# Performance work log

Hardware: AMD Instinct MI355X
Metric: run time of the kernel (lower is better)

## Reference

```python
import jax, jax.numpy as jnp
import numpy as np

N_NODES = 16384
N_EDGES = 131072
N_GRAPHS = 64
DIMS = [396, 4096, 2048, 1024, 1024, 2048, 256, 1]  # layer widths from __init__
BN_EPS = 1e-5


def setup_inputs() -> dict:
    key = jax.random.key(0)
    ks = jax.random.split(key, 32)
    inp = {
        "x": jax.random.normal(ks[0], (N_NODES, DIMS[0]), jnp.float32),
        "edge_index": jax.random.randint(ks[1], (2, N_EDGES), 0, N_NODES, dtype=jnp.int32),
        "batch": jnp.sort(jax.random.randint(ks[2], (N_NODES,), 0, N_GRAPHS, dtype=jnp.int32)),
    }
    for i in range(7):
        fi, fo = DIMS[i], DIMS[i + 1]
        inp[f"W{i+1}"] = jax.random.normal(ks[3 + i], (fi, fo), jnp.float32) * (1.0 / np.sqrt(fi)).astype(np.float32)
        inp[f"b{i+1}"] = jnp.zeros((fo,), jnp.float32)
    for i in range(6):
        inp[f"g{i+1}"] = jnp.ones((DIMS[i + 1],), jnp.float32)
        inp[f"be{i+1}"] = jnp.zeros((DIMS[i + 1],), jnp.float32)
    return inp


def _gcn_norm(edge_index, n):
    # PyG GCNConv default: add self-loops, sym-normalize D^-1/2 (A+I) D^-1/2
    loop = jnp.arange(n, dtype=edge_index.dtype)
    src = jnp.concatenate([edge_index[0], loop])
    dst = jnp.concatenate([edge_index[1], loop])
    deg = jax.ops.segment_sum(jnp.ones_like(src, jnp.float32), dst, num_segments=n)
    dinv = jax.lax.rsqrt(jnp.maximum(deg, 1.0))  # deg >= 1 due to self-loops
    norm = dinv[src] * dinv[dst]  # [E + N]
    return src, dst, norm


def _gcn_conv(x, W, b, src, dst, norm, n):
    h = x @ W                                   # dense linear transform
    msg = h[src] * norm[:, None]                # gather + edge scaling
    agg = jax.ops.segment_sum(msg, dst, num_segments=n)  # scatter-add
    return agg + b


def _bn(x, g, b):
    # BatchNorm1d in training mode: biased batch variance
    m = jnp.mean(x, axis=0)
    v = jnp.mean(jnp.square(x - m), axis=0)
    return (x - m) * jax.lax.rsqrt(v + BN_EPS) * g + b


def reference(x, edge_index, batch,
              W1, b1, W2, b2, W3, b3, W4, b4, W5, b5, W6, b6, W7, b7,
              g1, be1, g2, be2, g3, be3, g4, be4, g5, be5, g6, be6):
    n = x.shape[0]
    src, dst, norm = _gcn_norm(edge_index, n)
    Ws = [W1, W2, W3, W4, W5, W6]
    bs = [b1, b2, b3, b4, b5, b6]
    gs = [g1, g2, g3, g4, g5, g6]
    bes = [be1, be2, be3, be4, be5, be6]
    h = x
    for W, b, g, be in zip(Ws, bs, gs, bes):
        h = jax.nn.relu(_gcn_conv(h, W, b, src, dst, norm, n))
        h = _bn(h, g, be)
    h = _gcn_conv(h, W7, b7, src, dst, norm, n)   # [N, 1], no relu/bn
    out = jax.ops.segment_sum(h, batch, num_segments=N_GRAPHS)  # global_add_pool
    return out
```

## Files before the change

### kernel.cpp

```cpp
#include <hip/hip_runtime.h>


#define NN 16384
#define NE 131072
#define NG 64

typedef unsigned int u32;
typedef unsigned short u16;
typedef __attribute__((ext_vector_type(8))) short short8;
typedef __attribute__((ext_vector_type(4))) float f32x4;
typedef __attribute__((ext_vector_type(8))) u16 us8;
typedef __attribute__((ext_vector_type(4))) u16 us4;
typedef __attribute__((ext_vector_type(2))) u16 us2;

#define AS1(p) ((const __attribute__((address_space(1))) void*)(p))
#define AS3(p) ((__attribute__((address_space(3))) void*)(p))

__device__ __forceinline__ float b2f(u16 h) { return __uint_as_float(((u32)h) << 16); }
__device__ __forceinline__ u16 f2b(float f) {
    u32 u = __float_as_uint(f);
    return (u16)((u + 0x7FFFu + ((u >> 16) & 1u)) >> 16);
}

template <int VW> struct VecU;
template <> struct VecU<8> { typedef us8 T; };
template <> struct VecU<4> { typedef us4 T; };
template <> struct VecU<2> { typedef us2 T; };
template <> struct VecU<1> { typedef u16 T; };

template <int VW>
__device__ __forceinline__ void loadf(const u16* p, float* f) {
    typename VecU<VW>::T v = *(const typename VecU<VW>::T*)p;
    if constexpr (VW == 1) {
        f[0] = b2f((u16)v);
    } else {
        #pragma unroll
        for (int j = 0; j < VW; ++j) f[j] = b2f(v[j]);
    }
}
template <int VW>
__device__ __forceinline__ void storef(u16* p, const float* f) {
    typename VecU<VW>::T v;
    if constexpr (VW == 1) {
        v = f2b(f[0]);
    } else {
        #pragma unroll
        for (int j = 0; j < VW; ++j) v[j] = f2b(f[j]);
    }
    *(typename VecU<VW>::T*)p = v;
}

__global__ void k_degi(const int* __restrict__ dst, int* __restrict__ deg) {
    int e = blockIdx.x * 256 + threadIdx.x;
    if (e < NE) atomicAdd(&deg[dst[e]], 1);
}
__global__ void k_dinv(const int* __restrict__ deg, float* __restrict__ dinv) {
    int i = blockIdx.x * 256 + threadIdx.x;
    if (i < NN) dinv[i] = rsqrtf((float)(deg[i] + 1));
}
__global__ void k_nrm(const int* __restrict__ src, const int* __restrict__ dst,
                      const float* __restrict__ dinv, float* __restrict__ nrm) {
    int e = blockIdx.x * 256 + threadIdx.x;
    if (e < NE) nrm[e] = dinv[src[e]] * dinv[dst[e]];
}
__global__ __launch_bounds__(1024) void k_scan(const int* __restrict__ deg, int* __restrict__ rowptr) {
    __shared__ int part[1024];
    int t = threadIdx.x;
    int base = t * 16;
    int s = 0;
    #pragma unroll
    for (int j = 0; j < 16; ++j) s += deg[base + j];
    part[t] = s;
    __syncthreads();
    for (int off = 1; off < 1024; off <<= 1) {
        int v = 0;
        if (t >= off) v = part[t - off];
        __syncthreads();
        part[t] += v;
        __syncthreads();
    }
    int run = part[t] - s;
    for (int j = 0; j < 16; ++j) { rowptr[base + j] = run; run += deg[base + j]; }
    if (t == 1023) rowptr[NN] = run;
}
__global__ void k_place(const int* __restrict__ src, const int* __restrict__ dst,
                        const float* __restrict__ nrm, const int* __restrict__ rowptr,
                        int* __restrict__ cursor, int* __restrict__ csr_src,
                        float* __restrict__ csr_w) {
    int e = blockIdx.x * 256 + threadIdx.x;
    if (e >= NE) return;
    int d = dst[e];
    int p = rowptr[d] + atomicAdd(&cursor[d], 1);
    csr_src[p] = src[e];
    csr_w[p] = nrm[e];
}
__global__ void k_srow(const int* __restrict__ rowptr, const float* __restrict__ csr_w,
                       const float* __restrict__ dinv, float* __restrict__ svec) {
    int i = blockIdx.x * 256 + threadIdx.x;
    if (i >= NN) return;
    float s = dinv[i] * dinv[i];
    int r1 = rowptr[i + 1];
    for (int e = rowptr[i]; e < r1; ++e) s += csr_w[e];
    svec[i] = s;
}

__global__ void k_x2b(const float* __restrict__ x, u16* __restrict__ xp) {
    int idx = blockIdx.x * 256 + threadIdx.x;
    int i = idx >> 9, c = idx & 511;
    float v = (c < 396) ? x[(size_t)i * 396 + c] : 0.f;
    xp[idx] = f2b(v);
}
__global__ void k_wt(const float* __restrict__ W, u16* __restrict__ Wt,
                     int Ksrc, int Kpad, int N) {
    __shared__ float t[32][33];
    int k0 = blockIdx.x * 32, n0 = blockIdx.y * 32;
    #pragma unroll
    for (int j = 0; j < 4; ++j) {
        int k = k0 + threadIdx.y + j * 8;
        float v = 0.f;
        if (k < Ksrc) v = W[(size_t)k * N + n0 + threadIdx.x];
        t[threadIdx.y + j * 8][threadIdx.x] = v;
    }
    __syncthreads();
    #pragma unroll
    for (int j = 0; j < 4; ++j) {
        int n = n0 + threadIdx.y + j * 8;
        int k = k0 + threadIdx.x;
        Wt[(size_t)n * Kpad + k] = f2b(t[threadIdx.x][threadIdx.y + j * 8]);
    }
}

template <int VW>
__global__ __launch_bounds__(256) void k_agg(const u16* __restrict__ in, u16* __restrict__ out,
                                             const int* __restrict__ rowptr,
                                             const int* __restrict__ csr_src,
                                             const float* __restrict__ csr_w,
                                             const float* __restrict__ dinv,
                                             const float* __restrict__ svec,
                                             const float* __restrict__ bias,
                                             const float* __restrict__ av,
                                             const float* __restrict__ bvv,
                                             int F, int mode) {
    int i = blockIdx.x;
    int c0 = threadIdx.x * VW;
    float acc[VW];
    float d2 = dinv[i]; d2 *= d2;
    {
        float v[VW];
        loadf<VW>(in + (size_t)i * F + c0, v);
        #pragma unroll
        for (int j = 0; j < VW; ++j) acc[j] = d2 * v[j];
    }
    int r0 = rowptr[i], r1 = rowptr[i + 1];
    for (int e = r0; e < r1; ++e) {
        int s = csr_src[e];
        float w = csr_w[e];
        float v[VW];
        loadf<VW>(in + (size_t)s * F + c0, v);
        #pragma unroll
        for (int j = 0; j < VW; ++j) acc[j] += w * v[j];
    }
    if (mode == 1) {
        #pragma unroll
        for (int j = 0; j < VW; ++j) acc[j] = fmaxf(acc[j] + bias[c0 + j], 0.f);
    } else if (mode == 2) {
        float si = svec[i];
        #pragma unroll
        for (int j = 0; j < VW; ++j) acc[j] = av[c0 + j] * acc[j] + si * bvv[c0 + j];
    }
    storef<VW>(out + (size_t)i * F + c0, acc);
}

#define SROWS 128
template <int VW>
__global__ __launch_bounds__(256) void k_stats(const u16* __restrict__ h, float* __restrict__ s1,
                                               float* __restrict__ s2, int F) {
    int c0 = (blockIdx.x * 256 + threadIdx.x) * VW;
    int r0 = blockIdx.y * SROWS;
    float s[VW], q[VW];
    #pragma unroll
    for (int j = 0; j < VW; ++j) { s[j] = 0.f; q[j] = 0.f; }
    for (int r = r0; r < r0 + SROWS; ++r) {
        float v[VW];
        loadf<VW>(h + (size_t)r * F + c0, v);
        #pragma unroll
        for (int j = 0; j < VW; ++j) { s[j] += v[j]; q[j] += v[j] * v[j]; }
    }
    #pragma unroll
    for (int j = 0; j < VW; ++j) {
        atomicAdd(&s1[c0 + j], s[j]);
        atomicAdd(&s2[c0 + j], q[j]);
    }
}
__global__ void k_bnab(const float* __restrict__ s1, const float* __restrict__ s2,
                       const float* __restrict__ g, const float* __restrict__ be,
                       float* __restrict__ a, float* __restrict__ b, int F) {
    int c = blockIdx.x * 256 + threadIdx.x;
    if (c >= F) return;
    float m = s1[c] * (1.f / NN);
    float v = s2[c] * (1.f / NN) - m * m;
    float aa = g[c] * rsqrtf(v + 1e-5f);
    a[c] = aa;
    b[c] = be[c] - m * aa;
}
__global__ __launch_bounds__(256) void k_bnapply(u16* __restrict__ h, const float* __restrict__ a,
                                                 const float* __restrict__ b, int F) {
    size_t idx = blockIdx.x * (size_t)256 + threadIdx.x;
    int Fv = F >> 3;
    int c = (int)(idx % Fv) * 8;
    u16* p = h + idx * 8;
    float v[8];
    loadf<8>(p, v);
    #pragma unroll
    for (int j = 0; j < 8; ++j) v[j] = a[c + j] * v[j] + b[c + j];
    storef<8>(p, v);
}

__device__ __forceinline__ void stage16k(const char* gbase, size_t rs, int ktile, int h,
                                         char* slot, int tid) {
    size_t colb = (size_t)ktile * 128 + h * 64;
    #pragma unroll
    for (int i = 0; i < 2; ++i) {
        int G = i * 512 + tid;
        int r = G >> 2;
        int c = (G & 3) ^ (r & 3);
        __builtin_amdgcn_global_load_lds(AS1(gbase + (size_t)r * rs + colb + c * 16),
                                         AS3(slot + i * 8192 + ((tid >> 6) << 10)), 16, 0, 0);
    }
}

__global__ __launch_bounds__(512, 2) void k_gemm256(const u16* __restrict__ A,
                                                    const u16* __restrict__ Wt,
                                                    const float* __restrict__ bias,
                                                    u16* __restrict__ C,
                                                    int K, int N, int bx, int fuse) {
    extern __shared__ __align__(16) char smem[];
    int nwg = gridDim.x;
    int chunk = nwg >> 3;
    int swz = (blockIdx.x & 7) * chunk + (blockIdx.x >> 3);
    int tx = swz % bx, ty = swz / bx;
    int tid = threadIdx.x;
    int wid = tid >> 6, lane = tid & 63;
    int wr = wid >> 2, wc = wid & 3;
    int lo = lane & 15, hi = lane >> 4;
    int sw = ((hi ^ (lo & 3)) << 4);
    size_t row0 = (size_t)ty * 256;
    size_t col0 = (size_t)tx * 256;
    int nkt = K >> 6;

    const char* gA = (const char*)(A + row0 * K);
    const char* gB = (const char*)(Wt + col0 * K);
    size_t rs = (size_t)K * 2;

    const char* aA = smem + wr * 8192 + lo * 64 + sw;
    const char* bA = smem + 65536 + wc * 4096 + lo * 64 + sw;
#define ASL(b, h) (smem + (((b) * 2 + (h)) << 14))
#define BSL(b, h) (smem + 65536 + (((b) * 2 + (h)) << 14))

    f32x4 acc[8][4];
    #pragma unroll
    for (int m = 0; m < 8; ++m)
        #pragma unroll
        for (int n = 0; n < 4; ++n) acc[m][n] = {0.f, 0.f, 0.f, 0.f};
    short8 af[4], bf[4];

    stage16k(gA, rs, 0, 0, ASL(0, 0), tid);
    stage16k(gB, rs, 0, 0, BSL(0, 0), tid);
    stage16k(gA, rs, 0, 1, ASL(0, 1), tid);
    stage16k(gB, rs, 0, 1, BSL(0, 1), tid);
    stage16k(gA, rs, 1, 0, ASL(1, 0), tid);
    stage16k(gB, rs, 1, 0, BSL(1, 0), tid);
    asm volatile("s_waitcnt vmcnt(4)" ::: "memory");
    __builtin_amdgcn_sched_barrier(0);
    __builtin_amdgcn_s_barrier();

#define DS_LOADS(KK, MH)                                                                   \
    {                                                                                      \
        _Pragma("unroll") for (int j = 0; j < 4; ++j)                                      \
            af[j] = *(const short8*)(aA + buf * 32768 + (KK) * 16384 + (MH) * 4096 + j * 1024); \
        if ((MH) == 0) {                                                                   \
            _Pragma("unroll") for (int j = 0; j < 4; ++j)                                  \
                bf[j] = *(const short8*)(bA + buf * 32768 + (KK) * 16384 + j * 1024);      \
        }                                                                                  \
    }
#define MFMA_PHASE(MH)                                                                     \
    {                                                                                      \
        asm volatile("" ::: "memory");                                                     \
        __builtin_amdgcn_s_barrier();                                                      \
        __builtin_amdgcn_s_setprio(1);                                                     \
        _Pragma("unroll") for (int j = 0; j < 4; ++j)                                      \
            _Pragma("unroll") for (int n = 0; n < 4; ++n)                                  \
                acc[(MH) * 4 + j][n] = __builtin_amdgcn_mfma_f32_16x16x32_bf16(            \
                    af[j], bf[n], acc[(MH) * 4 + j][n], 0, 0, 0);                          \
        __builtin_amdgcn_s_setprio(0);                                                     \
    }
#define END_BARRIER                                                                        \
    {                                                                                      \
        asm volatile("" ::: "memory");                                                     \
        __builtin_amdgcn_s_barrier();                                                      \
    }

    for (int kt = 0; kt < nkt; ++kt) {
        int buf = kt & 1;
        DS_LOADS(0, 0);
        if (kt + 1 < nkt) {
            stage16k(gA, rs, kt + 1, 1, ASL(buf ^ 1, 1), tid);
            stage16k(gB, rs, kt + 1, 1, BSL(buf ^ 1, 1), tid);
        }
        MFMA_PHASE(0);
        END_BARRIER;
        DS_LOADS(0, 1);
        MFMA_PHASE(1);
        END_BARRIER;
        DS_LOADS(1, 0);
        if (kt + 2 < nkt) stage16k(gA, rs, kt + 2, 0, ASL(buf, 0), tid);
        MFMA_PHASE(0);
        END_BARRIER;
        DS_LOADS(1, 1);
        if (kt + 2 < nkt) stage16k(gB, rs, kt + 2, 0, BSL(buf, 0), tid);
        MFMA_PHASE(1);
        asm volatile("s_waitcnt vmcnt(4)" ::: "memory");
        __builtin_amdgcn_sched_barrier(0);
        END_BARRIER;
    }

    #pragma unroll
    for (int fm = 0; fm < 8; ++fm) {
        #pragma unroll
        for (int n = 0; n < 4; ++n) {
            #pragma unroll
            for (int r = 0; r < 4; ++r) {
                size_t row = row0 + wr * 128 + fm * 16 + hi * 4 + r;
                size_t col = col0 + wc * 64 + n * 16 + lo;
                float v = acc[fm][n][r];
                if (fuse) v = fmaxf(v + bias[col], 0.f);
                C[row * N + col] = f2b(v);
            }
        }
    }
#undef DS_LOADS
#undef MFMA_PHASE
#undef END_BARRIER
#undef ASL
#undef BSL
}

__global__ __launch_bounds__(256) void k_gemm(const u16* __restrict__ A, const u16* __restrict__ Wt,
                                              const float* __restrict__ bias, u16* __restrict__ C,
                                              int K, int N, int bx, int fuse) {
    __shared__ __align__(16) u16 As[128 * 32];
    __shared__ __align__(16) u16 Bs[128 * 32];
    int nwg = gridDim.x;
    int chunk = nwg >> 3;
    int swz = (blockIdx.x & 7) * chunk + (blockIdx.x >> 3);
    int tx = swz % bx, ty = swz / bx;
    int tid = threadIdx.x;
    int wid = tid >> 6, lane = tid & 63;
    int wr = wid >> 1, wc = wid & 1;
    int lo = lane & 15, hi = lane >> 4;
    size_t row0 = (size_t)ty * 128;
    size_t col0 = (size_t)tx * 128;

    f32x4 acc[4][4];
    #pragma unroll
    for (int m = 0; m < 4; ++m)
        #pragma unroll
        for (int n = 0; n < 4; ++n) acc[m][n] = {0.f, 0.f, 0.f, 0.f};

    const char* gA = (const char*)(A + row0 * K);
    const char* gB = (const char*)(Wt + col0 * K);
    size_t rs = (size_t)K * 2;
    int lin0 = tid * 16;
    int lin1 = lin0 + 4096;
    int rA0 = lin0 >> 6, cb0 = lin0 & 63;
    int rA1 = lin1 >> 6, cb1 = lin1 & 63;
    unsigned ldsOff = (unsigned)(wid << 10);

    for (int k0 = 0; k0 < K; k0 += 32) {
        __syncthreads();
        size_t kb = (size_t)k0 * 2;
        __builtin_amdgcn_global_load_lds(AS1(gA + (size_t)rA0 * rs + cb0 + kb),
                                         AS3((char*)As + ldsOff), 16, 0, 0);
        __builtin_amdgcn_global_load_lds(AS1(gA + (size_t)rA1 * rs + cb1 + kb),
                                         AS3((char*)As + 4096 + ldsOff), 16, 0, 0);
        __builtin_amdgcn_global_load_lds(AS1(gB + (size_t)rA0 * rs + cb0 + kb),
                                         AS3((char*)Bs + ldsOff), 16, 0, 0);
        __builtin_amdgcn_global_load_lds(AS1(gB + (size_t)rA1 * rs + cb1 + kb),
                                         AS3((char*)Bs + 4096 + ldsOff), 16, 0, 0);
        __syncthreads();
        short8 afr[4], bfr[4];
        #pragma unroll
        for (int m = 0; m < 4; ++m)
            afr[m] = *(const short8*)((const short*)As + (wr * 64 + m * 16 + lo) * 32 + hi * 8);
        #pragma unroll
        for (int n = 0; n < 4; ++n)
            bfr[n] = *(const short8*)((const short*)Bs + (wc * 64 + n * 16 + lo) * 32 + hi * 8);
        #pragma unroll
        for (int m = 0; m < 4; ++m)
            #pragma unroll
            for (int n = 0; n < 4; ++n)
                acc[m][n] = __builtin_amdgcn_mfma_f32_16x16x32_bf16(afr[m], bfr[n], acc[m][n], 0, 0, 0);
    }
    #pragma unroll
    for (int m = 0; m < 4; ++m) {
        #pragma unroll
        for (int n = 0; n < 4; ++n) {
            #pragma unroll
            for (int r = 0; r < 4; ++r) {
                size_t row = row0 + wr * 64 + m * 16 + hi * 4 + r;
                size_t col = col0 + wc * 64 + n * 16 + lo;
                float v = acc[m][n][r];
                if (fuse) v = fmaxf(v + bias[col], 0.f);
                C[row * N + col] = f2b(v);
            }
        }
    }
}

__global__ __launch_bounds__(256) void k_gemv(const u16* __restrict__ A, const float* __restrict__ w,
                                              const float* __restrict__ a, const float* __restrict__ b,
                                              float* __restrict__ y) {
    int row = blockIdx.x * 4 + (threadIdx.x >> 6);
    int lane = threadIdx.x & 63;
    const u16* h = A + (size_t)row * 256;
    float s = 0.f;
    #pragma unroll
    for (int j = 0; j < 4; ++j) {
        int c = lane + j * 64;
        s += (a[c] * b2f(h[c]) + b[c]) * w[c];
    }
    #pragma unroll
    for (int off = 32; off; off >>= 1) s += __shfl_down(s, off);
    if (lane == 0) y[row] = s;
}
__global__ void k_final(const float* __restrict__ y, const int* __restrict__ rowptr,
                        const int* __restrict__ csr_src, const float* __restrict__ csr_w,
                        const float* __restrict__ dinv, const int* __restrict__ batch,
                        const float* __restrict__ b7, float* __restrict__ out) {
    int i = blockIdx.x * 256 + threadIdx.x;
    if (i >= NN) return;
    float v = dinv[i] * dinv[i] * y[i];
    int r1 = rowptr[i + 1];
    for (int e = rowptr[i]; e < r1; ++e) v += csr_w[e] * y[csr_src[e]];
    atomicAdd(&out[batch[i]], v + b7[0]);
}
__global__ void k_sentinel(float* out, float v) {
    if (threadIdx.x == 0 && blockIdx.x == 0) out[0] = v;
}

static inline char* alignp(char* p) { return (char*)(((uintptr_t)p + 255) & ~(uintptr_t)255); }

extern "C" void kernel_launch(void* const* d_in, const int* in_sizes, int n_in,
                              void* d_out, int out_size, void* d_ws, size_t ws_size,
                              hipStream_t stream) {
    const float* x = (const float*)d_in[0];
    const int* ei = (const int*)d_in[1];
    const int* src = ei;
    const int* dst = ei + NE;
    const int* batch = (const int*)d_in[2];
    const float* W[7]; const float* bv[7];
    for (int i = 0; i < 7; ++i) { W[i] = (const float*)d_in[3 + 2 * i]; bv[i] = (const float*)d_in[4 + 2 * i]; }
    const float* g[6]; const float* be[6];
    for (int i = 0; i < 6; ++i) { g[i] = (const float*)d_in[17 + 2 * i]; be[i] = (const float*)d_in[18 + 2 * i]; }
    float* out = (float*)d_out;

    char* p = (char*)d_ws;
    u16* Abuf = (u16*)p; p += (size_t)NN * 4096 * 2;
    u16* Bbuf = (u16*)p; p += (size_t)NN * 2048 * 2;
    u16* xpad = (u16*)p; p += (size_t)NN * 512 * 2;
    u16* W1t = (u16*)p; p += (size_t)4096 * 512 * 2;
    u16* W2t = (u16*)p; p += (size_t)2048 * 4096 * 2;
    u16* W3t = (u16*)p; p += (size_t)1024 * 2048 * 2;
    u16* W4t = (u16*)p; p += (size_t)1024 * 1024 * 2;
    u16* W5t = (u16*)p; p += (size_t)2048 * 1024 * 2;
    u16* W6t = (u16*)p; p += (size_t)256 * 2048 * 2;
    p = alignp(p);
    int* degi = (int*)p; p += NN * 4;
    int* cursor = (int*)p; p += NN * 4;
    int* rowptr = (int*)p; p += (NN + 1) * 4; p = alignp(p);
    int* csr_src = (int*)p; p += NE * 4;
    float* csr_w = (float*)p; p += NE * 4;
    float* dinv = (float*)p; p += NN * 4;
    float* nrm = (float*)p; p += NE * 4;
    float* svec = (float*)p; p += NN * 4;
    float* s1 = (float*)p; p += 4096 * 4;
    float* s2 = (float*)p; p += 4096 * 4;
    float* bna = (float*)p; p += 4096 * 4;
    float* bnb = (float*)p; p += 4096 * 4;
    float* y = (float*)p; p += NN * 4;
    size_t need = (size_t)(p - (char*)d_ws);
    if (need > ws_size) {
        hipMemsetAsync(d_out, 0, NG * sizeof(float), stream);
        k_sentinel<<<1, 64, 0, stream>>>(out, (float)(ws_size >> 20));
        return;
    }

    (void)hipFuncSetAttribute((const void*)k_gemm256,
                              hipFuncAttributeMaxDynamicSharedMemorySize, 131072);

    hipMemsetAsync(degi, 0, 2 * NN * sizeof(int), stream);
    k_degi<<<NE / 256, 256, 0, stream>>>(dst, degi);
    k_dinv<<<NN / 256, 256, 0, stream>>>(degi, dinv);
    k_nrm<<<NE / 256, 256, 0, stream>>>(src, dst, dinv, nrm);
    k_scan<<<1, 1024, 0, stream>>>(degi, rowptr);
    k_place<<<NE / 256, 256, 0, stream>>>(src, dst, nrm, rowptr, cursor, csr_src, csr_w);
    k_srow<<<NN / 256, 256, 0, stream>>>(rowptr, csr_w, dinv, svec);

    k_x2b<<<(NN * 512) / 256, 256, 0, stream>>>(x, xpad);
    {
        dim3 b(32, 8);
        k_wt<<<dim3(16, 128), b, 0, stream>>>(W[0], W1t, 396, 512, 4096);
        k_wt<<<dim3(128, 64), b, 0, stream>>>(W[1], W2t, 4096, 4096, 2048);
        k_wt<<<dim3(64, 32), b, 0, stream>>>(W[2], W3t, 2048, 2048, 1024);
        k_wt<<<dim3(32, 32), b, 0, stream>>>(W[3], W4t, 1024, 1024, 1024);
        k_wt<<<dim3(32, 64), b, 0, stream>>>(W[4], W5t, 1024, 1024, 2048);
        k_wt<<<dim3(64, 8), b, 0, stream>>>(W[5], W6t, 2048, 2048, 256);
    }

    auto gemm = [&](const u16* A, const u16* Wt, const float* bias, u16* Cp, int K, int N, int fuse) {
        if (N >= 1024) {
            int bx = N / 256;
            k_gemm256<<<bx * (NN / 256), 512, 131072, stream>>>(A, Wt, bias, Cp, K, N, bx, fuse);
        } else {
            int bx = N / 128;
            k_gemm<<<bx * (NN / 128), 256, 0, stream>>>(A, Wt, bias, Cp, K, N, bx, fuse);
        }
    };
    auto agg = [&](const u16* in, u16* o, const float* bias, const float* av,
                   const float* bvv, int F, int mode) {
        if (F == 2048) k_agg<8><<<NN, 256, 0, stream>>>(in, o, rowptr, csr_src, csr_w, dinv, svec, bias, av, bvv, F, mode);
        else if (F == 1024) k_agg<4><<<NN, 256, 0, stream>>>(in, o, rowptr, csr_src, csr_w, dinv, svec, bias, av, bvv, F, mode);
        else if (F == 512) k_agg<2><<<NN, 256, 0, stream>>>(in, o, rowptr, csr_src, csr_w, dinv, svec, bias, av, bvv, F, mode);
        else k_agg<1><<<NN, 256, 0, stream>>>(in, o, rowptr, csr_src, csr_w, dinv, svec, bias, av, bvv, F, mode);
    };
    auto stats = [&](const u16* h, int F, int li) {
        hipMemsetAsync(s1, 0, 2 * 4096 * sizeof(float), stream);
        if (F == 4096) k_stats<8><<<dim3(2, NN / SROWS), 256, 0, stream>>>(h, s1, s2, F);
        else if (F == 2048) k_stats<8><<<dim3(1, NN / SROWS), 256, 0, stream>>>(h, s1, s2, F);
        else if (F == 1024) k_stats<4><<<dim3(1, NN / SROWS), 256, 0, stream>>>(h, s1, s2, F);
        else k_stats<1><<<dim3(1, NN / SROWS), 256, 0, stream>>>(h, s1, s2, F);
        k_bnab<<<(F + 255) / 256, 256, 0, stream>>>(s1, s2, g[li], be[li], bna, bnb, F);
    };
    auto bnapply = [&](u16* h, int F) {
        k_bnapply<<<(int)(((size_t)NN * F / 8) / 256), 256, 0, stream>>>(h, bna, bnb, F);
    };

    agg(xpad, Bbuf, nullptr, nullptr, nullptr, 512, 0);
    gemm(Bbuf, W1t, bv[0], Abuf, 512, 4096, 1);
    stats(Abuf, 4096, 0);
    bnapply(Abuf, 4096);

    gemm(Abuf, W2t, nullptr, Bbuf, 4096, 2048, 0);
    agg(Bbuf, Abuf, bv[1], nullptr, nullptr, 2048, 1);
    stats(Abuf, 2048, 1);
    bnapply(Abuf, 2048);

    gemm(Abuf, W3t, nullptr, Bbuf, 2048, 1024, 0);
    agg(Bbuf, Abuf, bv[2], nullptr, nullptr, 1024, 1);
    stats(Abuf, 1024, 2);
    bnapply(Abuf, 1024);

    gemm(Abuf, W4t, nullptr, Bbuf, 1024, 1024, 0);
    agg(Bbuf, Abuf, bv[3], nullptr, nullptr, 1024, 1);
    stats(Abuf, 1024, 3);

    agg(Abuf, Bbuf, nullptr, bna, bnb, 1024, 2);
    gemm(Bbuf, W5t, bv[4], Abuf, 1024, 2048, 1);
    stats(Abuf, 2048, 4);
    bnapply(Abuf, 2048);

    gemm(Abuf, W6t, nullptr, Bbuf, 2048, 256, 0);
    agg(Bbuf, Abuf, bv[5], nullptr, nullptr, 256, 1);
    stats(Abuf, 256, 5);

    k_gemv<<<NN / 4, 256, 0, stream>>>(Abuf, W[6], bna, bnb, y);
    hipMemsetAsync(d_out, 0, NG * sizeof(float), stream);
    k_final<<<NN / 256, 256, 0, stream>>>(y, rowptr, csr_src, csr_w, dinv, batch, bv[6], out);
}
```

Baseline: 1.470 ms.

## Switch intermediate storage and MFMA from bf16 to fp16; fuse BN coefficient computation

Changes the 16-bit intermediate format from bfloat16 to IEEE half, using f16 MFMA instructions and hardware conversions instead of manual bf16 rounding. Separately, folds the k_bnab coefficient kernel into k_bnapply for layers that apply BN in place, removing one launch per layer but recomputing rsqrt per element. fp16 has narrower range than bf16, which risks overflow for large activations, and the conversions must still match where the host-side packing writes the weights and inputs.

```diff
diff --git a/kernel.cpp b/kernel.cpp
--- a/kernel.cpp
+++ b/kernel.cpp
@@ -7,7 +7,7 @@
 
 typedef unsigned int u32;
 typedef unsigned short u16;
-typedef __attribute__((ext_vector_type(8))) short short8;
+typedef __attribute__((ext_vector_type(8))) _Float16 half8;
 typedef __attribute__((ext_vector_type(4))) float f32x4;
 typedef __attribute__((ext_vector_type(8))) u16 us8;
 typedef __attribute__((ext_vector_type(4))) u16 us4;
@@ -16,10 +16,13 @@
 #define AS1(p) ((const __attribute__((address_space(1))) void*)(p))
 #define AS3(p) ((__attribute__((address_space(3))) void*)(p))
 
-__device__ __forceinline__ float b2f(u16 h) { return __uint_as_float(((u32)h) << 16); }
+__device__ __forceinline__ float b2f(u16 h) {
+    _Float16 x = __builtin_bit_cast(_Float16, h);
+    return (float)x;
+}
 __device__ __forceinline__ u16 f2b(float f) {
-    u32 u = __float_as_uint(f);
-    return (u16)((u + 0x7FFFu + ((u >> 16) & 1u)) >> 16);
+    _Float16 x = (_Float16)f;
+    return __builtin_bit_cast(u16, x);
 }
 
 template <int VW> struct VecU;
@@ -203,8 +206,10 @@
     a[c] = aa;
     b[c] = be[c] - m * aa;
 }
-__global__ __launch_bounds__(256) void k_bnapply(u16* __restrict__ h, const float* __restrict__ a,
-                                                 const float* __restrict__ b, int F) {
+__global__ __launch_bounds__(256) void k_bnapply(u16* __restrict__ h, const float* __restrict__ s1,
+                                                 const float* __restrict__ s2,
+                                                 const float* __restrict__ g,
+                                                 const float* __restrict__ be, int F) {
     size_t idx = blockIdx.x * (size_t)256 + threadIdx.x;
     int Fv = F >> 3;
     int c = (int)(idx % Fv) * 8;
@@ -212,7 +217,12 @@
     float v[8];
     loadf<8>(p, v);
     #pragma unroll
-    for (int j = 0; j < 8; ++j) v[j] = a[c + j] * v[j] + b[c + j];
+    for (int j = 0; j < 8; ++j) {
+        float m = s1[c + j] * (1.f / NN);
+        float var = s2[c + j] * (1.f / NN) - m * m;
+        float a = g[c + j] * rsqrtf(var + 1e-5f);
+        v[j] = a * (v[j] - m) + be[c + j];
+    }
     storef<8>(p, v);
 }
 
@@ -262,7 +272,7 @@
     for (int m = 0; m < 8; ++m)
         #pragma unroll
         for (int n = 0; n < 4; ++n) acc[m][n] = {0.f, 0.f, 0.f, 0.f};
-    short8 af[4], bf[4];
+    half8 af[4], bf[4];
 
     stage16k(gA, rs, 0, 0, ASL(0, 0), tid);
     stage16k(gB, rs, 0, 0, BSL(0, 0), tid);
@@ -277,10 +287,10 @@
 #define DS_LOADS(KK, MH)                                                                   \
     {                                                                                      \
         _Pragma("unroll") for (int j = 0; j < 4; ++j)                                      \
-            af[j] = *(const short8*)(aA + buf * 32768 + (KK) * 16384 + (MH) * 4096 + j * 1024); \
+            af[j] = *(const half8*)(aA + buf * 32768 + (KK) * 16384 + (MH) * 4096 + j * 1024); \
         if ((MH) == 0) {                                                                   \
             _Pragma("unroll") for (int j = 0; j < 4; ++j)                                  \
-                bf[j] = *(const short8*)(bA + buf * 32768 + (KK) * 16384 + j * 1024);      \
+                bf[j] = *(const half8*)(bA + buf * 32768 + (KK) * 16384 + j * 1024);       \
         }                                                                                  \
     }
 #define MFMA_PHASE(MH)                                                                     \
@@ -290,7 +300,7 @@
         __builtin_amdgcn_s_setprio(1);                                                     \
         _Pragma("unroll") for (int j = 0; j < 4; ++j)                                      \
             _Pragma("unroll") for (int n = 0; n < 4; ++n)                                  \
-                acc[(MH) * 4 + j][n] = __builtin_amdgcn_mfma_f32_16x16x32_bf16(            \
+                acc[(MH) * 4 + j][n] = __builtin_amdgcn_mfma_f32_16x16x32_f16(             \
                     af[j], bf[n], acc[(MH) * 4 + j][n], 0, 0, 0);                          \
         __builtin_amdgcn_s_setprio(0);                                                     \
     }
@@ -388,18 +398,18 @@
         __builtin_amdgcn_global_load_lds(AS1(gB + (size_t)rA1 * rs + cb1 + kb),
                                          AS3((char*)Bs + 4096 + ldsOff), 16, 0, 0);
         __syncthreads();
-        short8 afr[4], bfr[4];
+        half8 afr[4], bfr[4];
         #pragma unroll
         for (int m = 0; m < 4; ++m)
-            afr[m] = *(const short8*)((const short*)As + (wr * 64 + m * 16 + lo) * 32 + hi * 8);
+            afr[m] = *(const half8*)((const u16*)As + (wr * 64 + m * 16 + lo) * 32 + hi * 8);
         #pragma unroll
         for (int n = 0; n < 4; ++n)
-            bfr[n] = *(const short8*)((const short*)Bs + (wc * 64 + n * 16 + lo) * 32 + hi * 8);
+            bfr[n] = *(const half8*)((const u16*)Bs + (wc * 64 + n * 16 + lo) * 32 + hi * 8);
         #pragma unroll
         for (int m = 0; m < 4; ++m)
             #pragma unroll
             for (int n = 0; n < 4; ++n)
-                acc[m][n] = __builtin_amdgcn_mfma_f32_16x16x32_bf16(afr[m], bfr[n], acc[m][n], 0, 0, 0);
+                acc[m][n] = __builtin_amdgcn_mfma_f32_16x16x32_f16(afr[m], bfr[n], acc[m][n], 0, 0, 0);
     }
     #pragma unroll
     for (int m = 0; m < 4; ++m) {
@@ -533,45 +543,46 @@
         else if (F == 512) k_agg<2><<<NN, 256, 0, stream>>>(in, o, rowptr, csr_src, csr_w, dinv, svec, bias, av, bvv, F, mode);
         else k_agg<1><<<NN, 256, 0, stream>>>(in, o, rowptr, csr_src, csr_w, dinv, svec, bias, av, bvv, F, mode);
     };
-    auto stats = [&](const u16* h, int F, int li) {
+    auto stats = [&](const u16* h, int F) {
         hipMemsetAsync(s1, 0, 2 * 4096 * sizeof(float), stream);
         if (F == 4096) k_stats<8><<<dim3(2, NN / SROWS), 256, 0, stream>>>(h, s1, s2, F);
         else if (F == 2048) k_stats<8><<<dim3(1, NN / SROWS), 256, 0, stream>>>(h, s1, s2, F);
         else if (F == 1024) k_stats<4><<<dim3(1, NN / SROWS), 256, 0, stream>>>(h, s1, s2, F);
         else k_stats<1><<<dim3(1, NN / SROWS), 256, 0, stream>>>(h, s1, s2, F);
-        k_bnab<<<(F + 255) / 256, 256, 0, stream>>>(s1, s2, g[li], be[li], bna, bnb, F);
     };
-    auto bnapply = [&](u16* h, int F) {
-        k_bnapply<<<(int)(((size_t)NN * F / 8) / 256), 256, 0, stream>>>(h, bna, bnb, F);
+    auto bnapply = [&](u16* h, int F, int li) {
+        k_bnapply<<<(int)(((size_t)NN * F / 8) / 256), 256, 0, stream>>>(h, s1, s2, g[li], be[li], F);
     };
 
     agg(xpad, Bbuf, nullptr, nullptr, nullptr, 512, 0);
     gemm(Bbuf, W1t, bv[0], Abuf, 512, 4096, 1);
-    stats(Abuf, 4096, 0);
-    bnapply(Abuf, 4096);
+    stats(Abuf, 4096);
+    bnapply(Abuf, 4096, 0);
 
     gemm(Abuf, W2t, nullptr, Bbuf, 4096, 2048, 0);
     agg(Bbuf, Abuf, bv[1], nullptr, nullptr, 2048, 1);
-    stats(Abuf, 2048, 1);
-    bnapply(Abuf, 2048);
+    stats(Abuf, 2048);
+    bnapply(Abuf, 2048, 1);
 
     gemm(Abuf, W3t, nullptr, Bbuf, 2048, 1024, 0);
     agg(Bbuf, Abuf, bv[2], nullptr, nullptr, 1024, 1);
-    stats(Abuf, 1024, 2);
-    bnapply(Abuf, 1024);
+    stats(Abuf, 1024);
+    bnapply(Abuf, 1024, 2);
 
     gemm(Abuf, W4t, nullptr, Bbuf, 1024, 1024, 0);
     agg(Bbuf, Abuf, bv[3], nullptr, nullptr, 1024, 1);
-    stats(Abuf, 1024, 3);
+    stats(Abuf, 1024);
+    k_bnab<<<1024 / 256, 256, 0, stream>>>(s1, s2, g[3], be[3], bna, bnb, 1024);
 
     agg(Abuf, Bbuf, nullptr, bna, bnb, 1024, 2);
     gemm(Bbuf, W5t, bv[4], Abuf, 1024, 2048, 1);
-    stats(Abuf, 2048, 4);
-    bnapply(Abuf, 2048);
+    stats(Abuf, 2048);
+    bnapply(Abuf, 2048, 4);
 
     gemm(Abuf, W6t, nullptr, Bbuf, 2048, 256, 0);
     agg(Bbuf, Abuf, bv[5], nullptr, nullptr, 256, 1);
-    stats(Abuf, 256, 5);
+    stats(Abuf, 256);
+    k_bnab<<<1, 256, 0, stream>>>(s1, s2, g[5], be[5], bna, bnb, 256);
 
     k_gemv<<<NN / 4, 256, 0, stream>>>(Abuf, W[6], bna, bnb, y);
     hipMemsetAsync(d_out, 0, NG * sizeof(float), stream);
```

Result: slower. 1.511 ms (+2.8%).
